# Optimization experiments

Hardware: AMD Instinct MI355X
Metric: run time of the kernel (lower is better)

The kernel has to match this reference:

```python
import jax, jax.numpy as jnp
import numpy as np

HIDDEN = 2048
HEADS = 16
HEAD_DIM = HIDDEN // HEADS
ROPE_BASE = 10000.0


def apply_rope(x):
    # x: [B, H, S, d]  (Llama-style half-split RoPE)
    d = x.shape[-1]
    S = x.shape[-2]
    inv_freq = 1.0 / (ROPE_BASE ** (jnp.arange(0, d, 2, dtype=jnp.float32) / d))
    freqs = jnp.arange(S, dtype=jnp.float32)[:, None] * inv_freq[None, :]  # [S, d/2]
    cos = jnp.concatenate([jnp.cos(freqs), jnp.cos(freqs)], axis=-1)  # [S, d]
    sin = jnp.concatenate([jnp.sin(freqs), jnp.sin(freqs)], axis=-1)
    x1, x2 = jnp.split(x, 2, axis=-1)
    rot = jnp.concatenate([-x2, x1], axis=-1)
    return x * cos.astype(x.dtype) + rot * sin.astype(x.dtype)


def setup_inputs() -> dict:
    key = jax.random.key(0)
    ks = jax.random.split(key, 6)
    B, S = 4, 1024
    x = jax.random.normal(ks[0], (B, S, HIDDEN), dtype=jnp.float32)
    attention_mask = jnp.zeros((B, S), dtype=jnp.float32)  # additive mask
    scale = 1.0 / np.sqrt(HIDDEN)
    Wq = jax.random.normal(ks[1], (HIDDEN, HIDDEN), dtype=jnp.float32) * scale
    Wk = jax.random.normal(ks[2], (HIDDEN, HIDDEN), dtype=jnp.float32) * scale
    Wv = jax.random.normal(ks[3], (HIDDEN, HIDDEN), dtype=jnp.float32) * scale
    Wo = jax.random.normal(ks[4], (HIDDEN, HIDDEN), dtype=jnp.float32) * scale
    return {"x": x, "attention_mask": attention_mask, "Wq": Wq, "Wk": Wk, "Wv": Wv, "Wo": Wo}


def reference(x, attention_mask, Wq, Wk, Wv, Wo):
    B, S, D = x.shape
    H, d = HEADS, HEAD_DIM
    # projections (nn.Linear: y = x @ W.T, no bias)
    q = jnp.einsum('bsd,ed->bse', x, Wq).reshape(B, S, H, d).transpose(0, 2, 1, 3)
    k = jnp.einsum('bsd,ed->bse', x, Wk).reshape(B, S, H, d).transpose(0, 2, 1, 3)
    v = jnp.einsum('bsd,ed->bse', x, Wv).reshape(B, S, H, d).transpose(0, 2, 1, 3)
    q = apply_rope(q)
    k = apply_rope(k)
    scores = jnp.einsum('bhqd,bhkd->bhqk', q, k) / jnp.sqrt(jnp.float32(d))
    causal = jnp.where(jnp.tril(jnp.ones((S, S), dtype=bool)), 0.0, -jnp.inf).astype(scores.dtype)
    scores = scores + causal[None, None]
    scores = scores + attention_mask[:, None, None, :]
    attn_weights = jax.nn.softmax(scores, axis=-1)
    # dropout is identity in eval mode
    out = jnp.einsum('bhqk,bhkd->bhqd', attn_weights, v)
    out = out.transpose(0, 2, 1, 3).reshape(B, S, D)
    out = jnp.einsum('bsd,ed->bse', out, Wo)
    return (out, attn_weights)
```

## Files before the change

### kernel.cpp

```cpp
#include <hip/hip_runtime.h>
#include <hip/hip_bf16.h>


typedef __attribute__((ext_vector_type(8))) short bf16x8;
typedef __attribute__((ext_vector_type(4))) float f32x4;

#define GLD_LDS16(g, l)                                                      \
  __builtin_amdgcn_global_load_lds(                                          \
      (const __attribute__((address_space(1))) unsigned int*)(g),            \
      (__attribute__((address_space(3))) unsigned int*)(l), 16, 0, 0)

__global__ __launch_bounds__(256) void cast_all(
    const float* __restrict__ x, const float* __restrict__ Wq,
    const float* __restrict__ Wk, const float* __restrict__ Wv,
    const float* __restrict__ Wo, __hip_bfloat16* __restrict__ ws) {
  int idx = blockIdx.x * 256 + threadIdx.x;
  const float* src;
  __hip_bfloat16* dst;
  int off;
  if (idx < 1048576) {
    src = x; dst = ws + 4194304; off = idx;
  } else if (idx < 1572864) {
    src = Wq; dst = ws + 12582912; off = idx - 1048576;
  } else if (idx < 2097152) {
    src = Wk; dst = ws + 16777216; off = idx - 1572864;
  } else if (idx < 2621440) {
    src = Wv; dst = ws + 20971520; off = idx - 2097152;
  } else {
    src = Wo; dst = ws; off = idx - 2621440;
  }
  const float4* p = (const float4*)src;
  float4 a = p[(size_t)off * 2], b = p[(size_t)off * 2 + 1];
  __hip_bfloat16 h[8] = {__float2bfloat16(a.x), __float2bfloat16(a.y),
                         __float2bfloat16(a.z), __float2bfloat16(a.w),
                         __float2bfloat16(b.x), __float2bfloat16(b.y),
                         __float2bfloat16(b.z), __float2bfloat16(b.w)};
  uint4 u;
  __builtin_memcpy(&u, h, 16);
  ((uint4*)dst)[off] = u;
}

__global__ __launch_bounds__(256) void gemm_qkv(
    const __hip_bfloat16* __restrict__ A, const __hip_bfloat16* __restrict__ W,
    __hip_bfloat16* __restrict__ QKV) {
  __shared__ alignas(16) __hip_bfloat16 lA[128][64];
  __shared__ alignas(16) __hip_bfloat16 lB[128][64];

  const int tid = threadIdx.x;
  const int m0 = blockIdx.y * 128;
  const int n0 = blockIdx.x * 128;
  const int z = blockIdx.z;
  const __hip_bfloat16* Bm = W + (size_t)z * (2048 * 2048);

  const int lane = tid & 63;
  const int wid = tid >> 6;
  const int wm = wid * 32;
  const int frow = lane & 15;
  const int fk = (lane >> 4) * 8;

  f32x4 acc[2][8] = {};

  for (int k0 = 0; k0 < 2048; k0 += 64) {
    __syncthreads();
#pragma unroll
    for (int c = 0; c < 4; ++c) {
      int lin = c * 256 + tid;
      int r = lin >> 3;
      int col = (lin & 7) << 3;
      GLD_LDS16(A + (size_t)(m0 + r) * 2048 + k0 + col, &lA[r][col]);
    }
#pragma unroll
    for (int c = 0; c < 4; ++c) {
      int lin = c * 256 + tid;
      int r = lin >> 3;
      int col = (lin & 7) << 3;
      GLD_LDS16(Bm + (size_t)(n0 + r) * 2048 + k0 + col, &lB[r][col]);
    }
    __syncthreads();
#pragma unroll
    for (int kk = 0; kk < 64; kk += 32) {
      bf16x8 av[2], bv[8];
#pragma unroll
      for (int i = 0; i < 2; ++i)
        av[i] = *(const bf16x8*)&lA[wm + i * 16 + frow][kk + fk];
#pragma unroll
      for (int i = 0; i < 8; ++i)
        bv[i] = *(const bf16x8*)&lB[i * 16 + frow][kk + fk];
#pragma unroll
      for (int mi = 0; mi < 2; ++mi)
#pragma unroll
        for (int ni = 0; ni < 8; ++ni)
          acc[mi][ni] = __builtin_amdgcn_mfma_f32_16x16x32_bf16(
              av[mi], bv[ni], acc[mi][ni], 0, 0, 0);
    }
  }

  const int r0 = (lane >> 4) * 4;
  const int cc = lane & 15;
  __hip_bfloat16* C = QKV + (size_t)z * (4096 * 2048);

  if (z < 2) {
    float invf[4];
#pragma unroll
    for (int ni = 0; ni < 4; ++ni)
      invf[ni] = __expf(-(float)(ni * 16 + cc) * 0.143911568312128f);
#pragma unroll
    for (int mi = 0; mi < 2; ++mi) {
#pragma unroll
      for (int rr = 0; rr < 4; ++rr) {
        int m = m0 + wm + mi * 16 + r0 + rr;
        float spos = (float)(m & 1023);
        __hip_bfloat16* crow = C + (size_t)m * 2048 + n0;
#pragma unroll
        for (int ni = 0; ni < 4; ++ni) {
          float sn, c;
          __sincosf(spos * invf[ni], &sn, &c);
          float x1 = acc[mi][ni][rr], x2 = acc[mi][ni + 4][rr];
          crow[ni * 16 + cc] = __float2bfloat16(x1 * c - x2 * sn);
          crow[(ni + 4) * 16 + cc] = __float2bfloat16(x2 * c + x1 * sn);
        }
      }
    }
  } else {
#pragma unroll
    for (int mi = 0; mi < 2; ++mi)
#pragma unroll
      for (int ni = 0; ni < 8; ++ni)
#pragma unroll
        for (int rr = 0; rr < 4; ++rr)
          C[(size_t)(m0 + wm + mi * 16 + r0 + rr) * 2048 +
            (n0 + ni * 16 + cc)] = __float2bfloat16(acc[mi][ni][rr]);
  }
}

template <int MODE>
__global__ __launch_bounds__(256) void gemm_nt(
    const __hip_bfloat16* __restrict__ Abase,
    const __hip_bfloat16* __restrict__ Bbase, float* __restrict__ Cbase) {
  __shared__ alignas(16) __hip_bfloat16 lA[128][64];
  __shared__ alignas(16) __hip_bfloat16 lB[128][64];

  const int tid = threadIdx.x;
  const int m0 = blockIdx.y * 128;
  const int n0 = blockIdx.x * 128;
  const int z = blockIdx.z;

  const __hip_bfloat16* A;
  const __hip_bfloat16* Bm;
  int K = 2048;
  if constexpr (MODE == 1) {
    if (n0 > m0) return;
    int b = z >> 4, h = z & 15;
    A = Abase + ((size_t)b * 1024) * 2048 + h * 128;
    Bm = Bbase + ((size_t)b * 1024) * 2048 + h * 128;
    K = 128;
  } else {
    A = Abase;
    Bm = Bbase;
  }

  const int lane = tid & 63;
  const int wid = tid >> 6;
  const int wm = (wid & 1) * 64;
  const int wn = (wid >> 1) * 64;
  const int frow = lane & 15;
  const int fk = (lane >> 4) * 8;

  f32x4 acc[4][4] = {};

  for (int k0 = 0; k0 < K; k0 += 64) {
    __syncthreads();
#pragma unroll
    for (int c = 0; c < 4; ++c) {
      int lin = c * 256 + tid;
      int r = lin >> 3;
      int col = (lin & 7) << 3;
      GLD_LDS16(A + (size_t)(m0 + r) * 2048 + k0 + col, &lA[r][col]);
    }
#pragma unroll
    for (int c = 0; c < 4; ++c) {
      int lin = c * 256 + tid;
      int r = lin >> 3;
      int col = (lin & 7) << 3;
      GLD_LDS16(Bm + (size_t)(n0 + r) * 2048 + k0 + col, &lB[r][col]);
    }
    __syncthreads();
#pragma unroll
    for (int kk = 0; kk < 64; kk += 32) {
      bf16x8 av[4], bv[4];
#pragma unroll
      for (int i = 0; i < 4; ++i)
        av[i] = *(const bf16x8*)&lA[wm + i * 16 + frow][kk + fk];
#pragma unroll
      for (int i = 0; i < 4; ++i)
        bv[i] = *(const bf16x8*)&lB[wn + i * 16 + frow][kk + fk];
#pragma unroll
      for (int mi = 0; mi < 4; ++mi)
#pragma unroll
        for (int ni = 0; ni < 4; ++ni)
          acc[mi][ni] = __builtin_amdgcn_mfma_f32_16x16x32_bf16(
              av[mi], bv[ni], acc[mi][ni], 0, 0, 0);
    }
  }

  const int r0 = (lane >> 4) * 4;
  const int cc = lane & 15;

  if constexpr (MODE == 1) {
    float* C = Cbase + (size_t)z * (1024 * 1024);
    const float scale = 0.08838834764831845f;
#pragma unroll
    for (int mi = 0; mi < 4; ++mi)
#pragma unroll
      for (int ni = 0; ni < 4; ++ni)
#pragma unroll
        for (int r = 0; r < 4; ++r)
          C[(size_t)(m0 + wm + mi * 16 + r0 + r) * 1024 +
            (n0 + wn + ni * 16 + cc)] = acc[mi][ni][r] * scale;
  } else {
#pragma unroll
    for (int mi = 0; mi < 4; ++mi)
#pragma unroll
      for (int ni = 0; ni < 4; ++ni)
#pragma unroll
        for (int r = 0; r < 4; ++r)
          Cbase[(size_t)(m0 + wm + mi * 16 + r0 + r) * 2048 +
                (n0 + wn + ni * 16 + cc)] = acc[mi][ni][r];
  }
}

__global__ __launch_bounds__(256) void gemm_pv(
    float* __restrict__ Sb, const __hip_bfloat16* __restrict__ Vt,
    const float* __restrict__ mask, __hip_bfloat16* __restrict__ AO) {
  __shared__ alignas(16) __hip_bfloat16 lA[128][64];
  __shared__ alignas(16) __hip_bfloat16 lB[128][64];

  const int tid = threadIdx.x;
  const int z = blockIdx.x;
  const int m0 = (7 - blockIdx.y) * 128;
  const int b = z >> 4, h = z & 15;
  float* S = Sb + (size_t)z * (1024 * 1024);
  const __hip_bfloat16* Bm = Vt + (size_t)z * (128 * 1024);
  const float* mrow = mask + b * 1024;
  const int K = m0 + 128;

  const int sr = tid >> 4;
  const int scol = (tid & 15) << 2;

  float mx[8], sm[8];
#pragma unroll
  for (int c = 0; c < 8; ++c) { mx[c] = -3.0e38f; sm[c] = 0.f; }

  for (int k0 = 0; k0 < K; k0 += 64) {
    float4 mk = *(const float4*)&mrow[k0 + scol];
#pragma unroll
    for (int c = 0; c < 8; ++c) {
      int r = c * 16 + sr;
      int i = m0 + r;
      float4 v = *(const float4*)&S[(size_t)i * 1024 + k0 + scol];
      float s[4] = {v.x + mk.x, v.y + mk.y, v.z + mk.z, v.w + mk.w};
      int j = k0 + scol;
#pragma unroll
      for (int e = 0; e < 4; ++e)
        if (j + e > i) s[e] = -3.0e38f;
      float tm = fmaxf(fmaxf(s[0], s[1]), fmaxf(s[2], s[3]));
      if (tm > mx[c]) {
        sm[c] *= __expf(mx[c] - tm);
        mx[c] = tm;
      }
#pragma unroll
      for (int e = 0; e < 4; ++e)
        sm[c] += (s[e] > -1.0e38f) ? __expf(s[e] - mx[c]) : 0.f;
    }
  }

  float inv[8];
#pragma unroll
  for (int c = 0; c < 8; ++c) {
#pragma unroll
    for (int off = 1; off < 16; off <<= 1) {
      float om = __shfl_xor(mx[c], off, 64);
      float os = __shfl_xor(sm[c], off, 64);
      float nm = fmaxf(mx[c], om);
      sm[c] = sm[c] * __expf(mx[c] - nm) + os * __expf(om - nm);
      mx[c] = nm;
    }
    inv[c] = 1.0f / sm[c];
  }

  const int lane = tid & 63;
  const int wid = tid >> 6;
  const int wm = (wid & 1) * 64;
  const int wn = (wid >> 1) * 64;
  const int frow = lane & 15;
  const int fk = (lane >> 4) * 8;

  f32x4 acc[4][4] = {};

  for (int k0 = K - 64; k0 >= 0; k0 -= 64) {
    __syncthreads();
    float4 mk = *(const float4*)&mrow[k0 + scol];
#pragma unroll
    for (int c = 0; c < 8; ++c) {
      int r = c * 16 + sr;
      int i = m0 + r;
      size_t soff = (size_t)i * 1024 + k0 + scol;
      float4 v = *(const float4*)&S[soff];
      float s[4] = {v.x + mk.x, v.y + mk.y, v.z + mk.z, v.w + mk.w};
      int j = k0 + scol;
      float w[4];
#pragma unroll
      for (int e = 0; e < 4; ++e)
        w[e] = (j + e <= i && s[e] > -1.0e38f) ? __expf(s[e] - mx[c]) * inv[c]
                                               : 0.f;
      float4 o = {w[0], w[1], w[2], w[3]};
      *(float4*)&S[soff] = o;
      __hip_bfloat16 hh[4] = {__float2bfloat16(w[0]), __float2bfloat16(w[1]),
                              __float2bfloat16(w[2]), __float2bfloat16(w[3])};
      unsigned long long u;
      __builtin_memcpy(&u, hh, 8);
      *(unsigned long long*)&lA[r][scol] = u;
    }
#pragma unroll
    for (int c = 0; c < 4; ++c) {
      int lin = c * 256 + tid;
      int r = lin >> 3;
      int col = (lin & 7) << 3;
      GLD_LDS16(Bm + (size_t)r * 1024 + k0 + col, &lB[r][col]);
    }
    __syncthreads();
#pragma unroll
    for (int kk = 0; kk < 64; kk += 32) {
      bf16x8 av[4], bv[4];
#pragma unroll
      for (int i = 0; i < 4; ++i)
        av[i] = *(const bf16x8*)&lA[wm + i * 16 + frow][kk + fk];
#pragma unroll
      for (int i = 0; i < 4; ++i)
        bv[i] = *(const bf16x8*)&lB[wn + i * 16 + frow][kk + fk];
#pragma unroll
      for (int mi = 0; mi < 4; ++mi)
#pragma unroll
        for (int ni = 0; ni < 4; ++ni)
          acc[mi][ni] = __builtin_amdgcn_mfma_f32_16x16x32_bf16(
              av[mi], bv[ni], acc[mi][ni], 0, 0, 0);
    }
  }

  const int r0 = (lane >> 4) * 4;
  const int cc = lane & 15;
  __hip_bfloat16* C = AO + ((size_t)b * 1024) * 2048 + h * 128;
#pragma unroll
  for (int mi = 0; mi < 4; ++mi)
#pragma unroll
    for (int ni = 0; ni < 4; ++ni)
#pragma unroll
      for (int r = 0; r < 4; ++r)
        C[(size_t)(m0 + wm + mi * 16 + r0 + r) * 2048 +
          (wn + ni * 16 + cc)] = __float2bfloat16(acc[mi][ni][r]);
}

__global__ __launch_bounds__(256) void transpose_v(
    const __hip_bfloat16* __restrict__ Vb, __hip_bfloat16* __restrict__ Vt) {
  __shared__ short t[64][65];
  int s0 = blockIdx.x * 64;
  int j0 = blockIdx.y * 64;
  int bh = blockIdx.z;
  int b = bh >> 4, h = bh & 15;
  const short* src = (const short*)(Vb + ((size_t)b * 1024) * 2048 + h * 128);
#pragma unroll
  for (int it = 0; it < 2; ++it) {
    int lin = it * 256 + threadIdx.x;
    int r = lin >> 3, c8 = (lin & 7) * 8;
    bf16x8 v = *(const bf16x8*)&src[(size_t)(s0 + r) * 2048 + j0 + c8];
#pragma unroll
    for (int e = 0; e < 8; ++e) t[r][c8 + e] = v[e];
  }
  __syncthreads();
  short* dst = (short*)(Vt + ((size_t)bh * 128 + j0) * 1024 + s0);
#pragma unroll
  for (int it = 0; it < 2; ++it) {
    int lin = it * 256 + threadIdx.x;
    int r2 = lin >> 3, c8 = (lin & 7) * 8;
    bf16x8 w;
#pragma unroll
    for (int e = 0; e < 8; ++e) w[e] = t[c8 + e][r2];
    *(bf16x8*)&dst[(size_t)r2 * 1024 + c8] = w;
  }
}

extern "C" void kernel_launch(void* const* d_in, const int* in_sizes, int n_in,
                              void* d_out, int out_size, void* d_ws,
                              size_t ws_size, hipStream_t stream) {
  const float* x = (const float*)d_in[0];
  const float* mask = (const float*)d_in[1];
  const float* Wq = (const float*)d_in[2];
  const float* Wk = (const float*)d_in[3];
  const float* Wv = (const float*)d_in[4];
  const float* Wo = (const float*)d_in[5];
  float* out = (float*)d_out;
  float* attnw = out + (size_t)4 * 1024 * 2048;

  __hip_bfloat16* wsb = (__hip_bfloat16*)d_ws;
  __hip_bfloat16* Wob = wsb;
  __hip_bfloat16* xb  = wsb + 4194304;
  __hip_bfloat16* Wqb = wsb + 12582912;
  __hip_bfloat16* Qb  = wsb + 25165824;
  __hip_bfloat16* Kb  = wsb + 33554432;
  __hip_bfloat16* Vb  = wsb + 41943040;
  __hip_bfloat16* Vt  = wsb + 50331648;
  __hip_bfloat16* AO  = wsb + 4194304;

  cast_all<<<12288, 256, 0, stream>>>(x, Wq, Wk, Wv, Wo, wsb);
  gemm_qkv<<<dim3(16, 32, 3), 256, 0, stream>>>(xb, Wqb, Qb);
  transpose_v<<<dim3(16, 2, 64), 256, 0, stream>>>(Vb, Vt);
  gemm_nt<1><<<dim3(8, 8, 64), 256, 0, stream>>>(Qb, Kb, attnw);
  gemm_pv<<<dim3(64, 8), 256, 0, stream>>>(attnw, Vt, mask, AO);
  gemm_nt<3><<<dim3(16, 32, 1), 256, 0, stream>>>(AO, Wob, out);
}
```

Baseline: 716.2 us.

## Fuse QK^T, softmax and PV into a flash-style attention kernel

Replaces the separate score GEMM and the softmax+PV kernel with one kernel that recomputes Q·K^T per tile in a stats pass and again in a normalize pass. Scores are never materialized in fp32; only the final attention weights are written once and then read back to build the bf16 P tile. This removes several full passes over the large score matrix in global memory. In exchange it doubles the QK^T MFMA work, and it adds a global round-trip plus an extra barrier per tile for P.

```diff
diff --git a/kernel.cpp b/kernel.cpp
--- a/kernel.cpp
+++ b/kernel.cpp
@@ -133,31 +133,15 @@
   }
 }
 
-template <int MODE>
-__global__ __launch_bounds__(256) void gemm_nt(
-    const __hip_bfloat16* __restrict__ Abase,
-    const __hip_bfloat16* __restrict__ Bbase, float* __restrict__ Cbase) {
+__global__ __launch_bounds__(256) void gemm_out(
+    const __hip_bfloat16* __restrict__ A, const __hip_bfloat16* __restrict__ Bm,
+    float* __restrict__ Cbase) {
   __shared__ alignas(16) __hip_bfloat16 lA[128][64];
   __shared__ alignas(16) __hip_bfloat16 lB[128][64];
 
   const int tid = threadIdx.x;
   const int m0 = blockIdx.y * 128;
   const int n0 = blockIdx.x * 128;
-  const int z = blockIdx.z;
-
-  const __hip_bfloat16* A;
-  const __hip_bfloat16* Bm;
-  int K = 2048;
-  if constexpr (MODE == 1) {
-    if (n0 > m0) return;
-    int b = z >> 4, h = z & 15;
-    A = Abase + ((size_t)b * 1024) * 2048 + h * 128;
-    Bm = Bbase + ((size_t)b * 1024) * 2048 + h * 128;
-    K = 128;
-  } else {
-    A = Abase;
-    Bm = Bbase;
-  }
 
   const int lane = tid & 63;
   const int wid = tid >> 6;
@@ -168,7 +152,7 @@
 
   f32x4 acc[4][4] = {};
 
-  for (int k0 = 0; k0 < K; k0 += 64) {
+  for (int k0 = 0; k0 < 2048; k0 += 64) {
     __syncthreads();
 #pragma unroll
     for (int c = 0; c < 4; ++c) {
@@ -205,159 +189,14 @@
 
   const int r0 = (lane >> 4) * 4;
   const int cc = lane & 15;
-
-  if constexpr (MODE == 1) {
-    float* C = Cbase + (size_t)z * (1024 * 1024);
-    const float scale = 0.08838834764831845f;
-#pragma unroll
-    for (int mi = 0; mi < 4; ++mi)
-#pragma unroll
-      for (int ni = 0; ni < 4; ++ni)
-#pragma unroll
-        for (int r = 0; r < 4; ++r)
-          C[(size_t)(m0 + wm + mi * 16 + r0 + r) * 1024 +
-            (n0 + wn + ni * 16 + cc)] = acc[mi][ni][r] * scale;
-  } else {
-#pragma unroll
-    for (int mi = 0; mi < 4; ++mi)
-#pragma unroll
-      for (int ni = 0; ni < 4; ++ni)
-#pragma unroll
-        for (int r = 0; r < 4; ++r)
-          Cbase[(size_t)(m0 + wm + mi * 16 + r0 + r) * 2048 +
-                (n0 + wn + ni * 16 + cc)] = acc[mi][ni][r];
-  }
-}
-
-__global__ __launch_bounds__(256) void gemm_pv(
-    float* __restrict__ Sb, const __hip_bfloat16* __restrict__ Vt,
-    const float* __restrict__ mask, __hip_bfloat16* __restrict__ AO) {
-  __shared__ alignas(16) __hip_bfloat16 lA[128][64];
-  __shared__ alignas(16) __hip_bfloat16 lB[128][64];
-
-  const int tid = threadIdx.x;
-  const int z = blockIdx.x;
-  const int m0 = (7 - blockIdx.y) * 128;
-  const int b = z >> 4, h = z & 15;
-  float* S = Sb + (size_t)z * (1024 * 1024);
-  const __hip_bfloat16* Bm = Vt + (size_t)z * (128 * 1024);
-  const float* mrow = mask + b * 1024;
-  const int K = m0 + 128;
-
-  const int sr = tid >> 4;
-  const int scol = (tid & 15) << 2;
-
-  float mx[8], sm[8];
-#pragma unroll
-  for (int c = 0; c < 8; ++c) { mx[c] = -3.0e38f; sm[c] = 0.f; }
-
-  for (int k0 = 0; k0 < K; k0 += 64) {
-    float4 mk = *(const float4*)&mrow[k0 + scol];
-#pragma unroll
-    for (int c = 0; c < 8; ++c) {
-      int r = c * 16 + sr;
-      int i = m0 + r;
-      float4 v = *(const float4*)&S[(size_t)i * 1024 + k0 + scol];
-      float s[4] = {v.x + mk.x, v.y + mk.y, v.z + mk.z, v.w + mk.w};
-      int j = k0 + scol;
-#pragma unroll
-      for (int e = 0; e < 4; ++e)
-        if (j + e > i) s[e] = -3.0e38f;
-      float tm = fmaxf(fmaxf(s[0], s[1]), fmaxf(s[2], s[3]));
-      if (tm > mx[c]) {
-        sm[c] *= __expf(mx[c] - tm);
-        mx[c] = tm;
-      }
-#pragma unroll
-      for (int e = 0; e < 4; ++e)
-        sm[c] += (s[e] > -1.0e38f) ? __expf(s[e] - mx[c]) : 0.f;
-    }
-  }
-
-  float inv[8];
-#pragma unroll
-  for (int c = 0; c < 8; ++c) {
-#pragma unroll
-    for (int off = 1; off < 16; off <<= 1) {
-      float om = __shfl_xor(mx[c], off, 64);
-      float os = __shfl_xor(sm[c], off, 64);
-      float nm = fmaxf(mx[c], om);
-      sm[c] = sm[c] * __expf(mx[c] - nm) + os * __expf(om - nm);
-      mx[c] = nm;
-    }
-    inv[c] = 1.0f / sm[c];
-  }
-
-  const int lane = tid & 63;
-  const int wid = tid >> 6;
-  const int wm = (wid & 1) * 64;
-  const int wn = (wid >> 1) * 64;
-  const int frow = lane & 15;
-  const int fk = (lane >> 4) * 8;
-
-  f32x4 acc[4][4] = {};
-
-  for (int k0 = K - 64; k0 >= 0; k0 -= 64) {
-    __syncthreads();
-    float4 mk = *(const float4*)&mrow[k0 + scol];
-#pragma unroll
-    for (int c = 0; c < 8; ++c) {
-      int r = c * 16 + sr;
-      int i = m0 + r;
-      size_t soff = (size_t)i * 1024 + k0 + scol;
-      float4 v = *(const float4*)&S[soff];
-      float s[4] = {v.x + mk.x, v.y + mk.y, v.z + mk.z, v.w + mk.w};
-      int j = k0 + scol;
-      float w[4];
-#pragma unroll
-      for (int e = 0; e < 4; ++e)
-        w[e] = (j + e <= i && s[e] > -1.0e38f) ? __expf(s[e] - mx[c]) * inv[c]
-                                               : 0.f;
-      float4 o = {w[0], w[1], w[2], w[3]};
-      *(float4*)&S[soff] = o;
-      __hip_bfloat16 hh[4] = {__float2bfloat16(w[0]), __float2bfloat16(w[1]),
-                              __float2bfloat16(w[2]), __float2bfloat16(w[3])};
-      unsigned long long u;
-      __builtin_memcpy(&u, hh, 8);
-      *(unsigned long long*)&lA[r][scol] = u;
-    }
-#pragma unroll
-    for (int c = 0; c < 4; ++c) {
-      int lin = c * 256 + tid;
-      int r = lin >> 3;
-      int col = (lin & 7) << 3;
-      GLD_LDS16(Bm + (size_t)r * 1024 + k0 + col, &lB[r][col]);
-    }
-    __syncthreads();
-#pragma unroll
-    for (int kk = 0; kk < 64; kk += 32) {
-      bf16x8 av[4], bv[4];
-#pragma unroll
-      for (int i = 0; i < 4; ++i)
-        av[i] = *(const bf16x8*)&lA[wm + i * 16 + frow][kk + fk];
-#pragma unroll
-      for (int i = 0; i < 4; ++i)
-        bv[i] = *(const bf16x8*)&lB[wn + i * 16 + frow][kk + fk];
-#pragma unroll
-      for (int mi = 0; mi < 4; ++mi)
-#pragma unroll
-        for (int ni = 0; ni < 4; ++ni)
-          acc[mi][ni] = __builtin_amdgcn_mfma_f32_16x16x32_bf16(
-              av[mi], bv[ni], acc[mi][ni], 0, 0, 0);
-    }
-  }
-
-  const int r0 = (lane >> 4) * 4;
-  const int cc = lane & 15;
-  __hip_bfloat16* C = AO + ((size_t)b * 1024) * 2048 + h * 128;
 #pragma unroll
   for (int mi = 0; mi < 4; ++mi)
 #pragma unroll
     for (int ni = 0; ni < 4; ++ni)
 #pragma unroll
       for (int r = 0; r < 4; ++r)
-        C[(size_t)(m0 + wm + mi * 16 + r0 + r) * 2048 +
-          (wn + ni * 16 + cc)] = __float2bfloat16(acc[mi][ni][r]);
+        Cbase[(size_t)(m0 + wm + mi * 16 + r0 + r) * 2048 +
+              (n0 + wn + ni * 16 + cc)] = acc[mi][ni][r];
 }
 
 __global__ __launch_bounds__(256) void transpose_v(
@@ -387,6 +226,215 @@
     for (int e = 0; e < 8; ++e) w[e] = t[c8 + e][r2];
     *(bf16x8*)&dst[(size_t)r2 * 1024 + c8] = w;
   }
+}
+
+__global__ __launch_bounds__(256) void flash_attn(
+    const __hip_bfloat16* __restrict__ Qb, const __hip_bfloat16* __restrict__ Kb,
+    const __hip_bfloat16* __restrict__ Vt, const float* __restrict__ mask,
+    float* __restrict__ Wout, __hip_bfloat16* __restrict__ AO) {
+  __shared__ alignas(16) __hip_bfloat16 lK[64][128];
+  __shared__ alignas(16) __hip_bfloat16 lV[128][64];
+  __shared__ alignas(16) __hip_bfloat16 lP[128][64];
+
+  const int tid = threadIdx.x;
+  const int ssel = blockIdx.x;
+  const int z = blockIdx.y;
+  const int m0 = (ssel & 1) ? ((ssel >> 1) * 128) : ((7 - (ssel >> 1)) * 128);
+  const int b = z >> 4, h = z & 15;
+  const int NT = (m0 + 128) >> 6;
+
+  const int lane = tid & 63;
+  const int wid = tid >> 6;
+  const int wm = wid * 32;
+  const int frow = lane & 15;
+  const int fk = (lane >> 4) * 8;
+  const int r0 = (lane >> 4) * 4;
+  const int cc = lane & 15;
+
+  const __hip_bfloat16* Qh = Qb + ((size_t)b * 1024) * 2048 + h * 128;
+  const __hip_bfloat16* Kh = Kb + ((size_t)b * 1024) * 2048 + h * 128;
+  const __hip_bfloat16* Vh = Vt + (size_t)z * (128 * 1024);
+  const float* mrow = mask + b * 1024;
+  float* Sv = Wout + (size_t)z * (1024 * 1024);
+  const float scale = 0.08838834764831845f;
+
+  bf16x8 qf[2][4];
+#pragma unroll
+  for (int mi = 0; mi < 2; ++mi)
+#pragma unroll
+    for (int kq = 0; kq < 4; ++kq)
+      qf[mi][kq] = *(const bf16x8*)
+          &Qh[(size_t)(m0 + wm + mi * 16 + frow) * 2048 + kq * 32 + fk];
+
+  float mx[2][4], sm[2][4];
+#pragma unroll
+  for (int mi = 0; mi < 2; ++mi)
+#pragma unroll
+    for (int rr = 0; rr < 4; ++rr) { mx[mi][rr] = -3.0e38f; sm[mi][rr] = 0.f; }
+
+  for (int t = 0; t < NT; ++t) {
+    const int j0 = t * 64;
+    __syncthreads();
+#pragma unroll
+    for (int c = 0; c < 4; ++c) {
+      int lin = c * 256 + tid;
+      int r = lin >> 4;
+      int col = (lin & 15) << 3;
+      GLD_LDS16(Kh + (size_t)(j0 + r) * 2048 + col, &lK[r][col]);
+    }
+    __syncthreads();
+    f32x4 as[2][4] = {};
+#pragma unroll
+    for (int kq = 0; kq < 4; ++kq) {
+      bf16x8 bk[4];
+#pragma unroll
+      for (int ni = 0; ni < 4; ++ni)
+        bk[ni] = *(const bf16x8*)&lK[ni * 16 + frow][kq * 32 + fk];
+#pragma unroll
+      for (int mi = 0; mi < 2; ++mi)
+#pragma unroll
+        for (int ni = 0; ni < 4; ++ni)
+          as[mi][ni] = __builtin_amdgcn_mfma_f32_16x16x32_bf16(
+              qf[mi][kq], bk[ni], as[mi][ni], 0, 0, 0);
+    }
+    float mk[4];
+#pragma unroll
+    for (int ni = 0; ni < 4; ++ni) mk[ni] = mrow[j0 + ni * 16 + cc];
+#pragma unroll
+    for (int mi = 0; mi < 2; ++mi) {
+#pragma unroll
+      for (int rr = 0; rr < 4; ++rr) {
+        const int i = m0 + wm + mi * 16 + r0 + rr;
+        float sv[4];
+        bool ok[4];
+#pragma unroll
+        for (int ni = 0; ni < 4; ++ni) {
+          int j = j0 + ni * 16 + cc;
+          ok[ni] = (j <= i);
+          sv[ni] = ok[ni] ? as[mi][ni][rr] * scale + mk[ni] : -3.0e38f;
+        }
+        float tm = fmaxf(fmaxf(sv[0], sv[1]), fmaxf(sv[2], sv[3]));
+        if (tm > mx[mi][rr]) {
+          sm[mi][rr] *= __expf(mx[mi][rr] - tm);
+          mx[mi][rr] = tm;
+        }
+#pragma unroll
+        for (int ni = 0; ni < 4; ++ni)
+          sm[mi][rr] += ok[ni] ? __expf(sv[ni] - mx[mi][rr]) : 0.f;
+      }
+    }
+  }
+
+  float inv[2][4];
+#pragma unroll
+  for (int mi = 0; mi < 2; ++mi) {
+#pragma unroll
+    for (int rr = 0; rr < 4; ++rr) {
+#pragma unroll
+      for (int off = 1; off < 16; off <<= 1) {
+        float om = __shfl_xor(mx[mi][rr], off, 64);
+        float os = __shfl_xor(sm[mi][rr], off, 64);
+        float nm = fmaxf(mx[mi][rr], om);
+        sm[mi][rr] = sm[mi][rr] * __expf(mx[mi][rr] - nm) + os * __expf(om - nm);
+        mx[mi][rr] = nm;
+      }
+      inv[mi][rr] = 1.0f / sm[mi][rr];
+    }
+  }
+
+  f32x4 acc[2][8] = {};
+  for (int t = 0; t < NT; ++t) {
+    const int j0 = t * 64;
+    __syncthreads();
+#pragma unroll
+    for (int c = 0; c < 4; ++c) {
+      int lin = c * 256 + tid;
+      int r = lin >> 4;
+      int col = (lin & 15) << 3;
+      GLD_LDS16(Kh + (size_t)(j0 + r) * 2048 + col, &lK[r][col]);
+    }
+#pragma unroll
+    for (int c = 0; c < 4; ++c) {
+      int lin = c * 256 + tid;
+      int r = lin >> 3;
+      int col = (lin & 7) << 3;
+      GLD_LDS16(Vh + (size_t)r * 1024 + j0 + col, &lV[r][col]);
+    }
+    __syncthreads();
+    f32x4 as[2][4] = {};
+#pragma unroll
+    for (int kq = 0; kq < 4; ++kq) {
+      bf16x8 bk[4];
+#pragma unroll
+      for (int ni = 0; ni < 4; ++ni)
+        bk[ni] = *(const bf16x8*)&lK[ni * 16 + frow][kq * 32 + fk];
+#pragma unroll
+      for (int mi = 0; mi < 2; ++mi)
+#pragma unroll
+        for (int ni = 0; ni < 4; ++ni)
+          as[mi][ni] = __builtin_amdgcn_mfma_f32_16x16x32_bf16(
+              qf[mi][kq], bk[ni], as[mi][ni], 0, 0, 0);
+    }
+    float mk[4];
+#pragma unroll
+    for (int ni = 0; ni < 4; ++ni) mk[ni] = mrow[j0 + ni * 16 + cc];
+#pragma unroll
+    for (int mi = 0; mi < 2; ++mi) {
+#pragma unroll
+      for (int rr = 0; rr < 4; ++rr) {
+        const int i = m0 + wm + mi * 16 + r0 + rr;
+#pragma unroll
+        for (int ni = 0; ni < 4; ++ni) {
+          int j = j0 + ni * 16 + cc;
+          float w = (j <= i)
+                        ? __expf(as[mi][ni][rr] * scale + mk[ni] - mx[mi][rr]) *
+                              inv[mi][rr]
+                        : 0.f;
+          Sv[(size_t)i * 1024 + j] = w;
+        }
+      }
+    }
+    __syncthreads();
+#pragma unroll
+    for (int c = 0; c < 8; ++c) {
+      int lin = c * 256 + tid;
+      int r = lin >> 4;
+      int col = (lin & 15) << 2;
+      float4 v = *(const float4*)&Sv[(size_t)(m0 + r) * 1024 + j0 + col];
+      __hip_bfloat16 hh[4] = {__float2bfloat16(v.x), __float2bfloat16(v.y),
+                              __float2bfloat16(v.z), __float2bfloat16(v.w)};
+      unsigned long long u;
+      __builtin_memcpy(&u, hh, 8);
+      *(unsigned long long*)&lP[r][col] = u;
+    }
+    __syncthreads();
+#pragma unroll
+    for (int kj = 0; kj < 64; kj += 32) {
+      bf16x8 av[2], bv[8];
+#pragma unroll
+      for (int mi = 0; mi < 2; ++mi)
+        av[mi] = *(const bf16x8*)&lP[wm + mi * 16 + frow][kj + fk];
+#pragma unroll
+      for (int ni = 0; ni < 8; ++ni)
+        bv[ni] = *(const bf16x8*)&lV[ni * 16 + frow][kj + fk];
+#pragma unroll
+      for (int mi = 0; mi < 2; ++mi)
+#pragma unroll
+        for (int ni = 0; ni < 8; ++ni)
+          acc[mi][ni] = __builtin_amdgcn_mfma_f32_16x16x32_bf16(
+              av[mi], bv[ni], acc[mi][ni], 0, 0, 0);
+    }
+  }
+
+  __hip_bfloat16* C = AO + ((size_t)b * 1024) * 2048 + h * 128;
+#pragma unroll
+  for (int mi = 0; mi < 2; ++mi)
+#pragma unroll
+    for (int ni = 0; ni < 8; ++ni)
+#pragma unroll
+      for (int rr = 0; rr < 4; ++rr)
+        C[(size_t)(m0 + wm + mi * 16 + r0 + rr) * 2048 + ni * 16 + cc] =
+            __float2bfloat16(acc[mi][ni][rr]);
 }
 
 extern "C" void kernel_launch(void* const* d_in, const int* in_sizes, int n_in,
@@ -414,7 +462,6 @@
   cast_all<<<12288, 256, 0, stream>>>(x, Wq, Wk, Wv, Wo, wsb);
   gemm_qkv<<<dim3(16, 32, 3), 256, 0, stream>>>(xb, Wqb, Qb);
   transpose_v<<<dim3(16, 2, 64), 256, 0, stream>>>(Vb, Vt);
-  gemm_nt<1><<<dim3(8, 8, 64), 256, 0, stream>>>(Qb, Kb, attnw);
-  gemm_pv<<<dim3(64, 8), 256, 0, stream>>>(attnw, Vt, mask, AO);
-  gemm_nt<3><<<dim3(16, 32, 1), 256, 0, stream>>>(AO, Wob, out);
-}
+  flash_attn<<<dim3(8, 64), 256, 0, stream>>>(Qb, Kb, Vt, mask, attnw, AO);
+  gemm_out<<<dim3(16, 32), 256, 0, stream>>>(AO, Wob, out);
+}
```

After: 779.7 us. 1.09x slower.

## Fuse V transpose into QKV epilogue and softmax stats into score GEMM

Applied to the files above, without the earlier changes.

The QKV GEMM epilogue now writes V directly in transposed per-head layout, so the separate transpose kernel is gone. The score GEMM also computes per-row partial max and sum-exp for each tile and writes them to a scratch buffer. The PV kernel merges these partials instead of re-reading the full score matrix in a first pass, which removes one full read of the large fp32 attention matrix. The costs are strided 8-byte transposed stores in the QKV epilogue, extra shuffle reductions in the score kernel, and a reused workspace region for the partials.

```diff
diff --git a/kernel.cpp b/kernel.cpp
--- a/kernel.cpp
+++ b/kernel.cpp
@@ -42,7 +42,7 @@
 
 __global__ __launch_bounds__(256) void gemm_qkv(
     const __hip_bfloat16* __restrict__ A, const __hip_bfloat16* __restrict__ W,
-    __hip_bfloat16* __restrict__ QKV) {
+    __hip_bfloat16* __restrict__ QKV, __hip_bfloat16* __restrict__ Vt) {
   __shared__ alignas(16) __hip_bfloat16 lA[128][64];
   __shared__ alignas(16) __hip_bfloat16 lB[128][64];
 
@@ -122,42 +122,43 @@
       }
     }
   } else {
-#pragma unroll
-    for (int mi = 0; mi < 2; ++mi)
-#pragma unroll
-      for (int ni = 0; ni < 8; ++ni)
-#pragma unroll
-        for (int rr = 0; rr < 4; ++rr)
-          C[(size_t)(m0 + wm + mi * 16 + r0 + rr) * 2048 +
-            (n0 + ni * 16 + cc)] = __float2bfloat16(acc[mi][ni][rr]);
-  }
-}
-
-template <int MODE>
-__global__ __launch_bounds__(256) void gemm_nt(
-    const __hip_bfloat16* __restrict__ Abase,
-    const __hip_bfloat16* __restrict__ Bbase, float* __restrict__ Cbase) {
+    const int hh = n0 >> 7;
+#pragma unroll
+    for (int mi = 0; mi < 2; ++mi) {
+      int m = m0 + wm + mi * 16 + r0;
+      int bb = m >> 10;
+      int s = m & 1023;
+      __hip_bfloat16* vdst = Vt + (((size_t)bb * 16 + hh) * 128) * 1024;
+#pragma unroll
+      for (int ni = 0; ni < 8; ++ni) {
+        int d = ni * 16 + cc;
+        __hip_bfloat16 hv[4] = {__float2bfloat16(acc[mi][ni][0]),
+                                __float2bfloat16(acc[mi][ni][1]),
+                                __float2bfloat16(acc[mi][ni][2]),
+                                __float2bfloat16(acc[mi][ni][3])};
+        unsigned long long u;
+        __builtin_memcpy(&u, hv, 8);
+        *(unsigned long long*)&vdst[(size_t)d * 1024 + s] = u;
+      }
+    }
+  }
+}
+
+__global__ __launch_bounds__(256) void gemm_scores(
+    const __hip_bfloat16* __restrict__ Qb, const __hip_bfloat16* __restrict__ Kb,
+    const float* __restrict__ mask, float* __restrict__ Cbase,
+    float* __restrict__ part) {
   __shared__ alignas(16) __hip_bfloat16 lA[128][64];
   __shared__ alignas(16) __hip_bfloat16 lB[128][64];
 
   const int tid = threadIdx.x;
   const int m0 = blockIdx.y * 128;
   const int n0 = blockIdx.x * 128;
+  if (n0 > m0) return;
   const int z = blockIdx.z;
-
-  const __hip_bfloat16* A;
-  const __hip_bfloat16* Bm;
-  int K = 2048;
-  if constexpr (MODE == 1) {
-    if (n0 > m0) return;
-    int b = z >> 4, h = z & 15;
-    A = Abase + ((size_t)b * 1024) * 2048 + h * 128;
-    Bm = Bbase + ((size_t)b * 1024) * 2048 + h * 128;
-    K = 128;
-  } else {
-    A = Abase;
-    Bm = Bbase;
-  }
+  const int b = z >> 4, h = z & 15;
+  const __hip_bfloat16* A = Qb + ((size_t)b * 1024) * 2048 + h * 128;
+  const __hip_bfloat16* Bm = Kb + ((size_t)b * 1024) * 2048 + h * 128;
 
   const int lane = tid & 63;
   const int wid = tid >> 6;
@@ -168,7 +169,7 @@
 
   f32x4 acc[4][4] = {};
 
-  for (int k0 = 0; k0 < K; k0 += 64) {
+  for (int k0 = 0; k0 < 128; k0 += 64) {
     __syncthreads();
 #pragma unroll
     for (int c = 0; c < 4; ++c) {
@@ -205,87 +206,96 @@
 
   const int r0 = (lane >> 4) * 4;
   const int cc = lane & 15;
-
-  if constexpr (MODE == 1) {
-    float* C = Cbase + (size_t)z * (1024 * 1024);
-    const float scale = 0.08838834764831845f;
-#pragma unroll
-    for (int mi = 0; mi < 4; ++mi)
+  const float scale = 0.08838834764831845f;
+  float* C = Cbase + (size_t)z * (1024 * 1024);
+
+#pragma unroll
+  for (int mi = 0; mi < 4; ++mi)
+#pragma unroll
+    for (int ni = 0; ni < 4; ++ni)
+#pragma unroll
+      for (int r = 0; r < 4; ++r)
+        C[(size_t)(m0 + wm + mi * 16 + r0 + r) * 1024 +
+          (n0 + wn + ni * 16 + cc)] = acc[mi][ni][r] * scale;
+
+  const float* mrow = mask + b * 1024;
+  float mk2[4];
+#pragma unroll
+  for (int ni = 0; ni < 4; ++ni) mk2[ni] = mrow[n0 + wn + ni * 16 + cc];
+  float2* p2 = (float2*)part +
+               (((((size_t)z * 8 + blockIdx.y) * 8 + blockIdx.x) * 2 +
+                 (wid >> 1))) * 128;
+#pragma unroll
+  for (int mi = 0; mi < 4; ++mi) {
+#pragma unroll
+    for (int r = 0; r < 4; ++r) {
+      const int i = m0 + wm + mi * 16 + r0 + r;
+      float sv[4];
+      bool ok[4];
+#pragma unroll
+      for (int ni = 0; ni < 4; ++ni) {
+        int j = n0 + wn + ni * 16 + cc;
+        ok[ni] = (j <= i);
+        sv[ni] = ok[ni] ? acc[mi][ni][r] * scale + mk2[ni] : -3.0e38f;
+      }
+      float lm = fmaxf(fmaxf(sv[0], sv[1]), fmaxf(sv[2], sv[3]));
+      float ls = 0.f;
 #pragma unroll
       for (int ni = 0; ni < 4; ++ni)
-#pragma unroll
-        for (int r = 0; r < 4; ++r)
-          C[(size_t)(m0 + wm + mi * 16 + r0 + r) * 1024 +
-            (n0 + wn + ni * 16 + cc)] = acc[mi][ni][r] * scale;
-  } else {
-#pragma unroll
-    for (int mi = 0; mi < 4; ++mi)
-#pragma unroll
-      for (int ni = 0; ni < 4; ++ni)
-#pragma unroll
-        for (int r = 0; r < 4; ++r)
-          Cbase[(size_t)(m0 + wm + mi * 16 + r0 + r) * 2048 +
-                (n0 + wn + ni * 16 + cc)] = acc[mi][ni][r];
+        ls += ok[ni] ? __expf(sv[ni] - lm) : 0.f;
+#pragma unroll
+      for (int off = 1; off < 16; off <<= 1) {
+        float om = __shfl_xor(lm, off, 64);
+        float os = __shfl_xor(ls, off, 64);
+        float nm = fmaxf(lm, om);
+        ls = ls * __expf(lm - nm) + os * __expf(om - nm);
+        lm = nm;
+      }
+      if (cc == 0) p2[wm + mi * 16 + r0 + r] = float2{lm, ls};
+    }
   }
 }
 
 __global__ __launch_bounds__(256) void gemm_pv(
     float* __restrict__ Sb, const __hip_bfloat16* __restrict__ Vt,
-    const float* __restrict__ mask, __hip_bfloat16* __restrict__ AO) {
+    const float* __restrict__ mask, const float* __restrict__ part,
+    __hip_bfloat16* __restrict__ AO) {
   __shared__ alignas(16) __hip_bfloat16 lA[128][64];
   __shared__ alignas(16) __hip_bfloat16 lB[128][64];
+  __shared__ float smx[128], sinv[128];
 
   const int tid = threadIdx.x;
   const int z = blockIdx.x;
-  const int m0 = (7 - blockIdx.y) * 128;
+  const int ytile = 7 - blockIdx.y;
+  const int m0 = ytile * 128;
   const int b = z >> 4, h = z & 15;
   float* S = Sb + (size_t)z * (1024 * 1024);
   const __hip_bfloat16* Bm = Vt + (size_t)z * (128 * 1024);
   const float* mrow = mask + b * 1024;
   const int K = m0 + 128;
 
+  if (tid < 128) {
+    const float2* pp =
+        (const float2*)part + ((size_t)z * 8 + ytile) * 16 * 128;
+    float m = -3.0e38f, s = 0.f;
+    for (int x = 0; x < 2 * (ytile + 1); ++x) {
+      float2 p = pp[x * 128 + tid];
+      float nm = fmaxf(m, p.x);
+      s = s * __expf(m - nm) + p.y * __expf(p.x - nm);
+      m = nm;
+    }
+    smx[tid] = m;
+    sinv[tid] = 1.0f / s;
+  }
+  __syncthreads();
+
   const int sr = tid >> 4;
   const int scol = (tid & 15) << 2;
-
-  float mx[8], sm[8];
-#pragma unroll
-  for (int c = 0; c < 8; ++c) { mx[c] = -3.0e38f; sm[c] = 0.f; }
-
-  for (int k0 = 0; k0 < K; k0 += 64) {
-    float4 mk = *(const float4*)&mrow[k0 + scol];
-#pragma unroll
-    for (int c = 0; c < 8; ++c) {
-      int r = c * 16 + sr;
-      int i = m0 + r;
-      float4 v = *(const float4*)&S[(size_t)i * 1024 + k0 + scol];
-      float s[4] = {v.x + mk.x, v.y + mk.y, v.z + mk.z, v.w + mk.w};
-      int j = k0 + scol;
-#pragma unroll
-      for (int e = 0; e < 4; ++e)
-        if (j + e > i) s[e] = -3.0e38f;
-      float tm = fmaxf(fmaxf(s[0], s[1]), fmaxf(s[2], s[3]));
-      if (tm > mx[c]) {
-        sm[c] *= __expf(mx[c] - tm);
-        mx[c] = tm;
-      }
-#pragma unroll
-      for (int e = 0; e < 4; ++e)
-        sm[c] += (s[e] > -1.0e38f) ? __expf(s[e] - mx[c]) : 0.f;
-    }
-  }
-
-  float inv[8];
+  float mx[8], inv[8];
 #pragma unroll
   for (int c = 0; c < 8; ++c) {
-#pragma unroll
-    for (int off = 1; off < 16; off <<= 1) {
-      float om = __shfl_xor(mx[c], off, 64);
-      float os = __shfl_xor(sm[c], off, 64);
-      float nm = fmaxf(mx[c], om);
-      sm[c] = sm[c] * __expf(mx[c] - nm) + os * __expf(om - nm);
-      mx[c] = nm;
-    }
-    inv[c] = 1.0f / sm[c];
+    mx[c] = smx[c * 16 + sr];
+    inv[c] = sinv[c * 16 + sr];
   }
 
   const int lane = tid & 63;
@@ -297,7 +307,7 @@
 
   f32x4 acc[4][4] = {};
 
-  for (int k0 = K - 64; k0 >= 0; k0 -= 64) {
+  for (int k0 = 0; k0 < K; k0 += 64) {
     __syncthreads();
     float4 mk = *(const float4*)&mrow[k0 + scol];
 #pragma unroll
@@ -360,33 +370,70 @@
           (wn + ni * 16 + cc)] = __float2bfloat16(acc[mi][ni][r]);
 }
 
-__global__ __launch_bounds__(256) void transpose_v(
-    const __hip_bfloat16* __restrict__ Vb, __hip_bfloat16* __restrict__ Vt) {
-  __shared__ short t[64][65];
-  int s0 = blockIdx.x * 64;
-  int j0 = blockIdx.y * 64;
-  int bh = blockIdx.z;
-  int b = bh >> 4, h = bh & 15;
-  const short* src = (const short*)(Vb + ((size_t)b * 1024) * 2048 + h * 128);
-#pragma unroll
-  for (int it = 0; it < 2; ++it) {
-    int lin = it * 256 + threadIdx.x;
-    int r = lin >> 3, c8 = (lin & 7) * 8;
-    bf16x8 v = *(const bf16x8*)&src[(size_t)(s0 + r) * 2048 + j0 + c8];
-#pragma unroll
-    for (int e = 0; e < 8; ++e) t[r][c8 + e] = v[e];
-  }
-  __syncthreads();
-  short* dst = (short*)(Vt + ((size_t)bh * 128 + j0) * 1024 + s0);
-#pragma unroll
-  for (int it = 0; it < 2; ++it) {
-    int lin = it * 256 + threadIdx.x;
-    int r2 = lin >> 3, c8 = (lin & 7) * 8;
-    bf16x8 w;
-#pragma unroll
-    for (int e = 0; e < 8; ++e) w[e] = t[c8 + e][r2];
-    *(bf16x8*)&dst[(size_t)r2 * 1024 + c8] = w;
-  }
+__global__ __launch_bounds__(256) void gemm_out(
+    const __hip_bfloat16* __restrict__ A, const __hip_bfloat16* __restrict__ Bm,
+    float* __restrict__ Cbase) {
+  __shared__ alignas(16) __hip_bfloat16 lA[128][64];
+  __shared__ alignas(16) __hip_bfloat16 lB[128][64];
+
+  const int tid = threadIdx.x;
+  const int m0 = blockIdx.y * 128;
+  const int n0 = blockIdx.x * 128;
+
+  const int lane = tid & 63;
+  const int wid = tid >> 6;
+  const int wm = (wid & 1) * 64;
+  const int wn = (wid >> 1) * 64;
+  const int frow = lane & 15;
+  const int fk = (lane >> 4) * 8;
+
+  f32x4 acc[4][4] = {};
+
+  for (int k0 = 0; k0 < 2048; k0 += 64) {
+    __syncthreads();
+#pragma unroll
+    for (int c = 0; c < 4; ++c) {
+      int lin = c * 256 + tid;
+      int r = lin >> 3;
+      int col = (lin & 7) << 3;
+      GLD_LDS16(A + (size_t)(m0 + r) * 2048 + k0 + col, &lA[r][col]);
+    }
+#pragma unroll
+    for (int c = 0; c < 4; ++c) {
+      int lin = c * 256 + tid;
+      int r = lin >> 3;
+      int col = (lin & 7) << 3;
+      GLD_LDS16(Bm + (size_t)(n0 + r) * 2048 + k0 + col, &lB[r][col]);
+    }
+    __syncthreads();
+#pragma unroll
+    for (int kk = 0; kk < 64; kk += 32) {
+      bf16x8 av[4], bv[4];
+#pragma unroll
+      for (int i = 0; i < 4; ++i)
+        av[i] = *(const bf16x8*)&lA[wm + i * 16 + frow][kk + fk];
+#pragma unroll
+      for (int i = 0; i < 4; ++i)
+        bv[i] = *(const bf16x8*)&lB[wn + i * 16 + frow][kk + fk];
+#pragma unroll
+      for (int mi = 0; mi < 4; ++mi)
+#pragma unroll
+        for (int ni = 0; ni < 4; ++ni)
+          acc[mi][ni] = __builtin_amdgcn_mfma_f32_16x16x32_bf16(
+              av[mi], bv[ni], acc[mi][ni], 0, 0, 0);
+    }
+  }
+
+  const int r0 = (lane >> 4) * 4;
+  const int cc = lane & 15;
+#pragma unroll
+  for (int mi = 0; mi < 4; ++mi)
+#pragma unroll
+    for (int ni = 0; ni < 4; ++ni)
+#pragma unroll
+      for (int r = 0; r < 4; ++r)
+        Cbase[(size_t)(m0 + wm + mi * 16 + r0 + r) * 2048 +
+              (n0 + wn + ni * 16 + cc)] = acc[mi][ni][r];
 }
 
 extern "C" void kernel_launch(void* const* d_in, const int* in_sizes, int n_in,
@@ -407,14 +454,13 @@
   __hip_bfloat16* Wqb = wsb + 12582912;
   __hip_bfloat16* Qb  = wsb + 25165824;
   __hip_bfloat16* Kb  = wsb + 33554432;
-  __hip_bfloat16* Vb  = wsb + 41943040;
   __hip_bfloat16* Vt  = wsb + 50331648;
   __hip_bfloat16* AO  = wsb + 4194304;
+  float* part = (float*)(wsb + 12582912);
 
   cast_all<<<12288, 256, 0, stream>>>(x, Wq, Wk, Wv, Wo, wsb);
-  gemm_qkv<<<dim3(16, 32, 3), 256, 0, stream>>>(xb, Wqb, Qb);
-  transpose_v<<<dim3(16, 2, 64), 256, 0, stream>>>(Vb, Vt);
-  gemm_nt<1><<<dim3(8, 8, 64), 256, 0, stream>>>(Qb, Kb, attnw);
-  gemm_pv<<<dim3(64, 8), 256, 0, stream>>>(attnw, Vt, mask, AO);
-  gemm_nt<3><<<dim3(16, 32, 1), 256, 0, stream>>>(AO, Wob, out);
-}
+  gemm_qkv<<<dim3(16, 32, 3), 256, 0, stream>>>(xb, Wqb, Qb, Vt);
+  gemm_scores<<<dim3(8, 8, 64), 256, 0, stream>>>(Qb, Kb, mask, attnw, part);
+  gemm_pv<<<dim3(64, 8), 256, 0, stream>>>(attnw, Vt, mask, part, AO);
+  gemm_out<<<dim3(16, 32), 256, 0, stream>>>(AO, Wob, out);
+}
```

Measured after the change: 768.6 us. +7.3%, slower.
